# Kernel optimization log

Hardware: AMD Instinct MI355X
Metric: run time of the kernel (lower is better)

The kernel has to match this reference:

```python
import jax, jax.numpy as jnp
import numpy as np

ND, NPROT, E, L = 20000, 8000, 640000, 200000
DD, DP, H = 128, 128, 256

PARAM_SHAPES = {
    # conv_in, per edge type (dp: drug->protein writes into protein; pd: reverse)
    'Wl_in_dp': (DD, H), 'bl_in_dp': (H,), 'Wr_in_dp': (DP, H),
    'Wl_in_pd': (DP, H), 'bl_in_pd': (H,), 'Wr_in_pd': (DD, H),
    # conv_med (shared across the 2 middle iterations)
    'Wl_med_dp': (H, H), 'bl_med_dp': (H,), 'Wr_med_dp': (H, H),
    'Wl_med_pd': (H, H), 'bl_med_pd': (H,), 'Wr_med_pd': (H, H),
    # conv_out
    'Wl_out_dp': (H, H), 'bl_out_dp': (H,), 'Wr_out_dp': (H, H),
    'Wl_out_pd': (H, H), 'bl_out_pd': (H,), 'Wr_out_pd': (H, H),
    # edge decoder MLP
    'W1': (2 * H, H), 'b1': (H,), 'W2': (H, 1), 'b2': (1,),
}


def setup_inputs() -> dict:
    key = jax.random.key(0)
    ks = jax.random.split(key, 6 + len(PARAM_SHAPES))
    def nrm(k, shape):
        return jax.random.normal(k, shape, dtype=jnp.float32) * 0.05
    inp = {
        'x_drug': nrm(ks[0], (ND, DD)),
        'x_prot': nrm(ks[1], (NPROT, DP)),
        'ei_src': jax.random.randint(ks[2], (E,), 0, ND, dtype=jnp.int32),
        'ei_dst': jax.random.randint(ks[3], (E,), 0, NPROT, dtype=jnp.int32),
        'eli_row': jax.random.randint(ks[4], (L,), 0, ND, dtype=jnp.int32),
        'eli_col': jax.random.randint(ks[5], (L,), 0, NPROT, dtype=jnp.int32),
    }
    for i, (name, sh) in enumerate(PARAM_SHAPES.items()):
        inp[name] = nrm(ks[6 + i], sh)
    return inp


def _sage(x_src, x_dst, src, dst, Wl, bl, Wr, n_dst):
    # SAGEConv(aggr='sum'): lin_l(scatter_sum over neighbors) + lin_r(x_dst)
    agg = jax.ops.segment_sum(x_src[src], dst, num_segments=n_dst)  # [n_dst, F]
    return agg @ Wl + bl + x_dst @ Wr


def reference(x_drug, x_prot, ei_src, ei_dst, eli_row, eli_col,
              Wl_in_dp, bl_in_dp, Wr_in_dp, Wl_in_pd, bl_in_pd, Wr_in_pd,
              Wl_med_dp, bl_med_dp, Wr_med_dp, Wl_med_pd, bl_med_pd, Wr_med_pd,
              Wl_out_dp, bl_out_dp, Wr_out_dp, Wl_out_pd, bl_out_pd, Wr_out_pd,
              W1, b1, W2, b2):
    def hetero_layer(xd, xp, Wl_dp, bl_dp, Wr_dp, Wl_pd, bl_pd, Wr_pd):
        zp = _sage(xd, xp, ei_src, ei_dst, Wl_dp, bl_dp, Wr_dp, NPROT)
        zd = _sage(xp, xd, ei_dst, ei_src, Wl_pd, bl_pd, Wr_pd, ND)
        return zd, zp

    # conv_in + tanh (dropout is identity in eval)
    xd, xp = hetero_layer(x_drug, x_prot, Wl_in_dp, bl_in_dp, Wr_in_dp,
                          Wl_in_pd, bl_in_pd, Wr_in_pd)
    xd, xp = jnp.tanh(xd), jnp.tanh(xp)
    # conv_med applied twice with shared weights
    for _ in range(2):
        xd, xp = hetero_layer(xd, xp, Wl_med_dp, bl_med_dp, Wr_med_dp,
                              Wl_med_pd, bl_med_pd, Wr_med_pd)
        xd, xp = jnp.tanh(xd), jnp.tanh(xp)
    # conv_out, no activation
    zd, zp = hetero_layer(xd, xp, Wl_out_dp, bl_out_dp, Wr_out_dp,
                          Wl_out_pd, bl_out_pd, Wr_out_pd)

    # edge decoder: gather pair embeddings -> 2-layer MLP
    z = jnp.concatenate([zd[eli_row], zp[eli_col]], axis=-1)  # [L, 2H]
    h = jax.nn.relu(z @ W1 + b1)
    out = (h @ W2 + b2).reshape(-1)  # [L]
    return (zd, zp, out)
```

## Files before the change

### kernel.cpp

```cpp
#include <hip/hip_runtime.h>
#include <hip/hip_bf16.h>

#define ND 20000
#define NP 8000
#define NE 640000
#define NL 200000
#define DD 128
#define HH 256

typedef __attribute__((ext_vector_type(8))) short short8;
typedef __attribute__((ext_vector_type(4))) float f32x4;

__device__ inline float bflo(unsigned int u) {
    union { unsigned int u; float f; } x; x.u = u << 16; return x.f;
}
__device__ inline float bfhi(unsigned int u) {
    union { unsigned int u; float f; } x; x.u = u & 0xffff0000u; return x.f;
}
__device__ inline unsigned short f2b(float f) {
    union { float f; unsigned int u; } x; x.f = f;
    unsigned int r = x.u + 0x7fffu + ((x.u >> 16) & 1u);
    return (unsigned short)(r >> 16);
}

__global__ void k_hist(const int* __restrict__ src, const int* __restrict__ dst,
                       int* __restrict__ deg_d, int* __restrict__ deg_p) {
    int i = blockIdx.x * blockDim.x + threadIdx.x;
    if (i < NE) {
        atomicAdd(&deg_p[dst[i]], 1);
        atomicAdd(&deg_d[src[i]], 1);
    }
}

__global__ void k_scan(const int* __restrict__ deg, int* __restrict__ rowptr,
                       int* __restrict__ cursor, int n) {
    __shared__ int s[1024];
    const int t = threadIdx.x;
    const int chunk = (n + 1023) / 1024;
    const int lo = t * chunk;
    const int hi = min(n, lo + chunk);
    int local = 0;
    for (int i = lo; i < hi; ++i) local += deg[i];
    s[t] = local;
    __syncthreads();
    for (int off = 1; off < 1024; off <<= 1) {
        int v = (t >= off) ? s[t - off] : 0;
        __syncthreads();
        s[t] += v;
        __syncthreads();
    }
    int base = s[t] - local;
    for (int i = lo; i < hi; ++i) {
        rowptr[i] = base;
        cursor[i] = base;
        base += deg[i];
    }
    if (t == 1023) rowptr[n] = s[1023];
}

__global__ void k_fill(const int* __restrict__ src, const int* __restrict__ dst,
                       int* __restrict__ cur_p, int* __restrict__ cur_d,
                       int* __restrict__ csr_p, int* __restrict__ csr_d) {
    int i = blockIdx.x * blockDim.x + threadIdx.x;
    if (i < NE) {
        int s = src[i], d = dst[i];
        csr_p[atomicAdd(&cur_p[d], 1)] = s;
        csr_d[atomicAdd(&cur_d[s], 1)] = d;
    }
}

__global__ void k_f2b(const float* __restrict__ in, unsigned short* __restrict__ out, int n4) {
    int i = blockIdx.x * blockDim.x + threadIdx.x;
    if (i < n4) {
        float4 v = ((const float4*)in)[i];
        ushort4 o;
        o.x = f2b(v.x); o.y = f2b(v.y); o.z = f2b(v.z); o.w = f2b(v.w);
        ((ushort4*)out)[i] = o;
    }
}

struct WtD { const float* src; unsigned short* dst; int kbits; };
struct WtPack { WtD d[14]; };
__global__ void k_wt(WtPack p) {
    WtD d = p.d[blockIdx.y];
    const int K = 1 << d.kbits;
    int i = blockIdx.x * blockDim.x + threadIdx.x;
    if (i < 256 * K) {
        int nn = i >> d.kbits, k = i & (K - 1);
        d.dst[i] = f2b(d.src[k * 256 + nn]);
    }
}

__global__ void k_agg128(const unsigned short* __restrict__ x, const int* __restrict__ rowptr,
                         const int* __restrict__ idx, unsigned short* __restrict__ agg) {
    const int b = blockIdx.x, t = threadIdx.x;
    const int s = rowptr[b], e = rowptr[b + 1];
    float a0 = 0.f, a1 = 0.f;
    int j = s;
    for (; j + 1 < e; j += 2) {
        unsigned int u = *(const unsigned int*)(x + (size_t)idx[j] * 128 + 2 * t);
        unsigned int v = *(const unsigned int*)(x + (size_t)idx[j + 1] * 128 + 2 * t);
        a0 += bflo(u) + bflo(v);
        a1 += bfhi(u) + bfhi(v);
    }
    if (j < e) {
        unsigned int u = *(const unsigned int*)(x + (size_t)idx[j] * 128 + 2 * t);
        a0 += bflo(u); a1 += bfhi(u);
    }
    agg[(size_t)b * 128 + 2 * t]     = f2b(a0);
    agg[(size_t)b * 128 + 2 * t + 1] = f2b(a1);
}

__global__ void k_agg256(const unsigned short* __restrict__ x, const int* __restrict__ rowptr,
                         const int* __restrict__ idx, unsigned short* __restrict__ agg) {
    const int b = blockIdx.x, t = threadIdx.x;
    const int s = rowptr[b], e = rowptr[b + 1];
    float a0 = 0.f, a1 = 0.f, a2 = 0.f, a3 = 0.f;
    int j = s;
    for (; j + 1 < e; j += 2) {
        uint2 u = *(const uint2*)(x + (size_t)idx[j] * 256 + 4 * t);
        uint2 v = *(const uint2*)(x + (size_t)idx[j + 1] * 256 + 4 * t);
        a0 += bflo(u.x) + bflo(v.x);
        a1 += bfhi(u.x) + bfhi(v.x);
        a2 += bflo(u.y) + bflo(v.y);
        a3 += bfhi(u.y) + bfhi(v.y);
    }
    if (j < e) {
        uint2 u = *(const uint2*)(x + (size_t)idx[j] * 256 + 4 * t);
        a0 += bflo(u.x); a1 += bfhi(u.x); a2 += bflo(u.y); a3 += bfhi(u.y);
    }
    agg[(size_t)b * 256 + 4 * t]     = f2b(a0);
    agg[(size_t)b * 256 + 4 * t + 1] = f2b(a1);
    agg[(size_t)b * 256 + 4 * t + 2] = f2b(a2);
    agg[(size_t)b * 256 + 4 * t + 3] = f2b(a3);
}

__global__ __launch_bounds__(256)
void k_mgemm(int n,
             const unsigned short* __restrict__ A1, const unsigned short* __restrict__ W1t, int K1,
             const unsigned short* __restrict__ A2, const unsigned short* __restrict__ W2t, int K2,
             const float* __restrict__ bias, float* __restrict__ outF,
             unsigned short* __restrict__ outB, int act) {
    __shared__ short As[64][40];
    __shared__ short Bs[128][40];

    const int tid = threadIdx.x;
    const int w = tid >> 6, l = tid & 63;
    const int m16 = l & 15, kg = l >> 4;
    const int row0 = blockIdx.x * 64;
    const int col0 = blockIdx.y * 128;

    const f32x4 z4 = {0.f, 0.f, 0.f, 0.f};
    f32x4 acc[4][2];
#pragma unroll
    for (int i = 0; i < 4; ++i)
#pragma unroll
        for (int j = 0; j < 2; ++j) acc[i][j] = z4;

    for (int pass = 0; pass < 2; ++pass) {
        const unsigned short* A  = pass ? A2 : A1;
        const unsigned short* Wt = pass ? W2t : W1t;
        const int K = pass ? K2 : K1;
        if (A == nullptr) continue;
        for (int k0 = 0; k0 < K; k0 += 32) {
            {
                const int ar = tid >> 2, ac = (tid & 3) * 8;
                const int gr = row0 + ar;
                short8 v = {0, 0, 0, 0, 0, 0, 0, 0};
                if (gr < n) v = *(const short8*)(A + (size_t)gr * K + k0 + ac);
                *(short8*)&As[ar][ac] = v;
                *(short8*)&Bs[ar][ac] =
                    *(const short8*)(Wt + (size_t)(col0 + ar) * K + k0 + ac);
                *(short8*)&Bs[ar + 64][ac] =
                    *(const short8*)(Wt + (size_t)(col0 + ar + 64) * K + k0 + ac);
            }
            __syncthreads();
            short8 af[4];
#pragma unroll
            for (int i = 0; i < 4; ++i) af[i] = *(const short8*)&As[16 * i + m16][8 * kg];
#pragma unroll
            for (int j = 0; j < 2; ++j) {
                short8 bf = *(const short8*)&Bs[32 * w + 16 * j + m16][8 * kg];
#pragma unroll
                for (int i = 0; i < 4; ++i)
                    acc[i][j] = __builtin_amdgcn_mfma_f32_16x16x32_bf16(af[i], bf, acc[i][j], 0, 0, 0);
            }
            __syncthreads();
        }
    }

#pragma unroll
    for (int j = 0; j < 2; ++j) {
        const int gc = col0 + 32 * w + 16 * j + m16;
        const float bv = bias ? bias[gc] : 0.f;
#pragma unroll
        for (int i = 0; i < 4; ++i) {
#pragma unroll
            for (int r = 0; r < 4; ++r) {
                const int gr = row0 + 16 * i + 4 * kg + r;
                if (gr < n) {
                    float v = acc[i][j][r] + bv;
                    if (act) v = tanhf(v);
                    if (outF) outF[(size_t)gr * HH + gc] = v;
                    if (outB) outB[(size_t)gr * HH + gc] = f2b(v);
                }
            }
        }
    }
}

__global__ void k_decode(const unsigned short* __restrict__ Ab, const unsigned short* __restrict__ Bb,
                         const int* __restrict__ rows, const int* __restrict__ cols,
                         const float* __restrict__ W2, const float* __restrict__ b2,
                         float* __restrict__ out) {
    const int wid = (blockIdx.x * blockDim.x + threadIdx.x) >> 6;
    const int lane = threadIdx.x & 63;
    if (wid >= NL) return;
    const int r = rows[wid], c = cols[wid];
    uint2 ua = *(const uint2*)(Ab + (size_t)r * HH + 4 * lane);
    uint2 ub = *(const uint2*)(Bb + (size_t)c * HH + 4 * lane);
    float4 wv = *(const float4*)(W2 + 4 * lane);
    float s = fmaxf(bflo(ua.x) + bflo(ub.x), 0.f) * wv.x +
              fmaxf(bfhi(ua.x) + bfhi(ub.x), 0.f) * wv.y +
              fmaxf(bflo(ua.y) + bflo(ub.y), 0.f) * wv.z +
              fmaxf(bfhi(ua.y) + bfhi(ub.y), 0.f) * wv.w;
#pragma unroll
    for (int off = 32; off > 0; off >>= 1) s += __shfl_xor(s, off, 64);
    if (lane == 0) out[wid] = s + b2[0];
}

extern "C" void kernel_launch(void* const* d_in, const int* in_sizes, int n_in,
                              void* d_out, int out_size, void* d_ws, size_t ws_size,
                              hipStream_t stream) {
    const float* x_drug  = (const float*)d_in[0];
    const float* x_prot  = (const float*)d_in[1];
    const int*   ei_src  = (const int*)d_in[2];
    const int*   ei_dst  = (const int*)d_in[3];
    const int*   eli_row = (const int*)d_in[4];
    const int*   eli_col = (const int*)d_in[5];
    const float* Wl_in_dp  = (const float*)d_in[6];
    const float* bl_in_dp  = (const float*)d_in[7];
    const float* Wr_in_dp  = (const float*)d_in[8];
    const float* Wl_in_pd  = (const float*)d_in[9];
    const float* bl_in_pd  = (const float*)d_in[10];
    const float* Wr_in_pd  = (const float*)d_in[11];
    const float* Wl_med_dp = (const float*)d_in[12];
    const float* bl_med_dp = (const float*)d_in[13];
    const float* Wr_med_dp = (const float*)d_in[14];
    const float* Wl_med_pd = (const float*)d_in[15];
    const float* bl_med_pd = (const float*)d_in[16];
    const float* Wr_med_pd = (const float*)d_in[17];
    const float* Wl_out_dp = (const float*)d_in[18];
    const float* bl_out_dp = (const float*)d_in[19];
    const float* Wr_out_dp = (const float*)d_in[20];
    const float* Wl_out_pd = (const float*)d_in[21];
    const float* bl_out_pd = (const float*)d_in[22];
    const float* Wr_out_pd = (const float*)d_in[23];
    const float* W1 = (const float*)d_in[24];
    const float* b1 = (const float*)d_in[25];
    const float* W2 = (const float*)d_in[26];
    const float* b2 = (const float*)d_in[27];

    char* ws = (char*)d_ws;
    size_t off = 0;
    auto alloc = [&](size_t bytes) {
        void* p = ws + off;
        off = (off + bytes + 255) & ~(size_t)255;
        return p;
    };

    int* deg_p    = (int*)alloc((size_t)NP * 4);
    int* deg_d    = (int*)alloc((size_t)ND * 4);
    int* rowptr_p = (int*)alloc((size_t)(NP + 1) * 4);
    int* rowptr_d = (int*)alloc((size_t)(ND + 1) * 4);
    int* cur_p    = (int*)alloc((size_t)NP * 4);
    int* cur_d    = (int*)alloc((size_t)ND * 4);
    int* csr_p    = (int*)alloc((size_t)NE * 4);
    int* csr_d    = (int*)alloc((size_t)NE * 4);

    unsigned short* wt[14];
    const int kk[14] = {128,128,128,128, 256,256,256,256, 256,256,256,256, 256,256};
    for (int i = 0; i < 14; ++i) wt[i] = (unsigned short*)alloc((size_t)256 * kk[i] * 2);

    unsigned short* xdbf = (unsigned short*)alloc((size_t)ND * DD * 2);
    unsigned short* xpbf = (unsigned short*)alloc((size_t)NP * DD * 2);
    unsigned short* xd_a = (unsigned short*)alloc((size_t)ND * HH * 2);
    unsigned short* xd_b = (unsigned short*)alloc((size_t)ND * HH * 2);
    unsigned short* xp_a = (unsigned short*)alloc((size_t)NP * HH * 2);
    unsigned short* xp_b = (unsigned short*)alloc((size_t)NP * HH * 2);
    unsigned short* aggd = (unsigned short*)alloc((size_t)ND * HH * 2);
    unsigned short* aggp = (unsigned short*)alloc((size_t)NP * HH * 2);
    unsigned short* zdbf = (unsigned short*)alloc((size_t)ND * HH * 2);
    unsigned short* zpbf = (unsigned short*)alloc((size_t)NP * HH * 2);

    float* zd   = (float*)d_out;
    float* zp   = zd + (size_t)ND * HH;
    float* outv = zp + (size_t)NP * HH;

    const dim3 gD((ND + 63) / 64, 2);
    const dim3 gP((NP + 63) / 64, 2);

    hipMemsetAsync(deg_p, 0, (size_t)NP * 4, stream);
    hipMemsetAsync(deg_d, 0, (size_t)ND * 4, stream);
    k_hist<<<(NE + 255) / 256, 256, 0, stream>>>(ei_src, ei_dst, deg_d, deg_p);
    k_scan<<<1, 1024, 0, stream>>>(deg_p, rowptr_p, cur_p, NP);
    k_scan<<<1, 1024, 0, stream>>>(deg_d, rowptr_d, cur_d, ND);
    k_fill<<<(NE + 255) / 256, 256, 0, stream>>>(ei_src, ei_dst, cur_p, cur_d, csr_p, csr_d);

    k_f2b<<<(ND * DD / 4 + 255) / 256, 256, 0, stream>>>(x_drug, xdbf, ND * DD / 4);
    k_f2b<<<(NP * DD / 4 + 255) / 256, 256, 0, stream>>>(x_prot, xpbf, NP * DD / 4);
    {
        WtPack p;
        const float* src[14] = {Wl_in_dp, Wr_in_dp, Wl_in_pd, Wr_in_pd,
                                Wl_med_dp, Wr_med_dp, Wl_med_pd, Wr_med_pd,
                                Wl_out_dp, Wr_out_dp, Wl_out_pd, Wr_out_pd,
                                W1, W1 + (size_t)HH * HH};
        for (int i = 0; i < 14; ++i) {
            p.d[i].src = src[i];
            p.d[i].dst = wt[i];
            p.d[i].kbits = (kk[i] == 128) ? 7 : 8;
        }
        k_wt<<<dim3(256, 14), 256, 0, stream>>>(p);
    }

    k_agg128<<<NP, 64, 0, stream>>>(xdbf, rowptr_p, csr_p, aggp);
    k_agg128<<<ND, 64, 0, stream>>>(xpbf, rowptr_d, csr_d, aggd);
    k_mgemm<<<gP, 256, 0, stream>>>(NP, aggp, wt[0], 128, xpbf, wt[1], 128, bl_in_dp, nullptr, xp_a, 1);
    k_mgemm<<<gD, 256, 0, stream>>>(ND, aggd, wt[2], 128, xdbf, wt[3], 128, bl_in_pd, nullptr, xd_a, 1);

    k_agg256<<<NP, 64, 0, stream>>>(xd_a, rowptr_p, csr_p, aggp);
    k_agg256<<<ND, 64, 0, stream>>>(xp_a, rowptr_d, csr_d, aggd);
    k_mgemm<<<gP, 256, 0, stream>>>(NP, aggp, wt[4], 256, xp_a, wt[5], 256, bl_med_dp, nullptr, xp_b, 1);
    k_mgemm<<<gD, 256, 0, stream>>>(ND, aggd, wt[6], 256, xd_a, wt[7], 256, bl_med_pd, nullptr, xd_b, 1);

    k_agg256<<<NP, 64, 0, stream>>>(xd_b, rowptr_p, csr_p, aggp);
    k_agg256<<<ND, 64, 0, stream>>>(xp_b, rowptr_d, csr_d, aggd);
    k_mgemm<<<gP, 256, 0, stream>>>(NP, aggp, wt[4], 256, xp_b, wt[5], 256, bl_med_dp, nullptr, xp_a, 1);
    k_mgemm<<<gD, 256, 0, stream>>>(ND, aggd, wt[6], 256, xd_b, wt[7], 256, bl_med_pd, nullptr, xd_a, 1);

    k_agg256<<<NP, 64, 0, stream>>>(xd_a, rowptr_p, csr_p, aggp);
    k_agg256<<<ND, 64, 0, stream>>>(xp_a, rowptr_d, csr_d, aggd);
    k_mgemm<<<gP, 256, 0, stream>>>(NP, aggp, wt[8], 256, xp_a, wt[9], 256, bl_out_dp, zp, zpbf, 0);
    k_mgemm<<<gD, 256, 0, stream>>>(ND, aggd, wt[10], 256, xd_a, wt[11], 256, bl_out_pd, zd, zdbf, 0);

    k_mgemm<<<gD, 256, 0, stream>>>(ND, zdbf, wt[12], 256, nullptr, nullptr, 0,
                                    nullptr, nullptr, xd_b, 0);
    k_mgemm<<<gP, 256, 0, stream>>>(NP, zpbf, wt[13], 256, nullptr, nullptr, 0,
                                    b1, nullptr, xp_b, 0);
    k_decode<<<(NL + 3) / 4, 256, 0, stream>>>(xd_b, xp_b, eli_row, eli_col, W2, b2, outv);
}
```

Baseline: 750.6 us.

## Batch drug/protein kernels into single launches and widen GEMM tile to full N

Merges the paired drug-side and protein-side launches (scan, f32-to-bf16 conversion, aggregation, GEMM) into single kernels that pick a side by block index, roughly halving the launch count. The GEMM tile also changes from 64x128 to 64x256, so each block covers all 256 output columns and the A tile is loaded once rather than twice. In exchange each block holds twice as many accumulators and twice the B shared-memory tile, which may reduce occupancy, and the GEMM grid shrinks to about 440 blocks.

```diff
diff --git a/kernel.cpp b/kernel.cpp
--- a/kernel.cpp
+++ b/kernel.cpp
@@ -32,9 +32,14 @@
     }
 }
 
-__global__ void k_scan(const int* __restrict__ deg, int* __restrict__ rowptr,
-                       int* __restrict__ cursor, int n) {
+__global__ void k_scan2(const int* __restrict__ degA, int* __restrict__ rowA,
+                        int* __restrict__ curA, int nA,
+                        const int* __restrict__ degB, int* __restrict__ rowB,
+                        int* __restrict__ curB, int nB) {
     __shared__ int s[1024];
+    const int* deg; int* rowptr; int* cursor; int n;
+    if (blockIdx.x == 0) { deg = degA; rowptr = rowA; cursor = curA; n = nA; }
+    else                 { deg = degB; rowptr = rowB; cursor = curB; n = nB; }
     const int t = threadIdx.x;
     const int chunk = (n + 1023) / 1024;
     const int lo = t * chunk;
@@ -69,13 +74,18 @@
     }
 }
 
-__global__ void k_f2b(const float* __restrict__ in, unsigned short* __restrict__ out, int n4) {
+__global__ void k_f2b2(const float* __restrict__ a, unsigned short* __restrict__ oa, int n4a,
+                       const float* __restrict__ b, unsigned short* __restrict__ ob, int n4b) {
     int i = blockIdx.x * blockDim.x + threadIdx.x;
-    if (i < n4) {
-        float4 v = ((const float4*)in)[i];
-        ushort4 o;
-        o.x = f2b(v.x); o.y = f2b(v.y); o.z = f2b(v.z); o.w = f2b(v.w);
-        ((ushort4*)out)[i] = o;
+    if (i < n4a) {
+        float4 v = ((const float4*)a)[i];
+        ushort4 o; o.x = f2b(v.x); o.y = f2b(v.y); o.z = f2b(v.z); o.w = f2b(v.w);
+        ((ushort4*)oa)[i] = o;
+    } else if (i - n4a < n4b) {
+        int j = i - n4a;
+        float4 v = ((const float4*)b)[j];
+        ushort4 o; o.x = f2b(v.x); o.y = f2b(v.y); o.z = f2b(v.z); o.w = f2b(v.w);
+        ((ushort4*)ob)[j] = o;
     }
 }
 
@@ -91,75 +101,86 @@
     }
 }
 
-__global__ void k_agg128(const unsigned short* __restrict__ x, const int* __restrict__ rowptr,
-                         const int* __restrict__ idx, unsigned short* __restrict__ agg) {
-    const int b = blockIdx.x, t = threadIdx.x;
-    const int s = rowptr[b], e = rowptr[b + 1];
+struct ASide { const unsigned short* x; const int* rowptr; const int* idx;
+               unsigned short* agg; int n; };
+
+__global__ void k_agg2_128(ASide s0, ASide s1) {
+    ASide S; int b;
+    int bi = blockIdx.x;
+    if (bi < s0.n) { S = s0; b = bi; } else { S = s1; b = bi - s0.n; }
+    const int t = threadIdx.x;
+    const int s = S.rowptr[b], e = S.rowptr[b + 1];
     float a0 = 0.f, a1 = 0.f;
     int j = s;
     for (; j + 1 < e; j += 2) {
-        unsigned int u = *(const unsigned int*)(x + (size_t)idx[j] * 128 + 2 * t);
-        unsigned int v = *(const unsigned int*)(x + (size_t)idx[j + 1] * 128 + 2 * t);
+        unsigned int u = *(const unsigned int*)(S.x + (size_t)S.idx[j] * 128 + 2 * t);
+        unsigned int v = *(const unsigned int*)(S.x + (size_t)S.idx[j + 1] * 128 + 2 * t);
         a0 += bflo(u) + bflo(v);
         a1 += bfhi(u) + bfhi(v);
     }
     if (j < e) {
-        unsigned int u = *(const unsigned int*)(x + (size_t)idx[j] * 128 + 2 * t);
+        unsigned int u = *(const unsigned int*)(S.x + (size_t)S.idx[j] * 128 + 2 * t);
         a0 += bflo(u); a1 += bfhi(u);
     }
-    agg[(size_t)b * 128 + 2 * t]     = f2b(a0);
-    agg[(size_t)b * 128 + 2 * t + 1] = f2b(a1);
-}
-
-__global__ void k_agg256(const unsigned short* __restrict__ x, const int* __restrict__ rowptr,
-                         const int* __restrict__ idx, unsigned short* __restrict__ agg) {
-    const int b = blockIdx.x, t = threadIdx.x;
-    const int s = rowptr[b], e = rowptr[b + 1];
+    S.agg[(size_t)b * 128 + 2 * t]     = f2b(a0);
+    S.agg[(size_t)b * 128 + 2 * t + 1] = f2b(a1);
+}
+
+__global__ void k_agg2_256(ASide s0, ASide s1) {
+    ASide S; int b;
+    int bi = blockIdx.x;
+    if (bi < s0.n) { S = s0; b = bi; } else { S = s1; b = bi - s0.n; }
+    const int t = threadIdx.x;
+    const int s = S.rowptr[b], e = S.rowptr[b + 1];
     float a0 = 0.f, a1 = 0.f, a2 = 0.f, a3 = 0.f;
     int j = s;
     for (; j + 1 < e; j += 2) {
-        uint2 u = *(const uint2*)(x + (size_t)idx[j] * 256 + 4 * t);
-        uint2 v = *(const uint2*)(x + (size_t)idx[j + 1] * 256 + 4 * t);
+        uint2 u = *(const uint2*)(S.x + (size_t)S.idx[j] * 256 + 4 * t);
+        uint2 v = *(const uint2*)(S.x + (size_t)S.idx[j + 1] * 256 + 4 * t);
         a0 += bflo(u.x) + bflo(v.x);
         a1 += bfhi(u.x) + bfhi(v.x);
         a2 += bflo(u.y) + bflo(v.y);
         a3 += bfhi(u.y) + bfhi(v.y);
     }
     if (j < e) {
-        uint2 u = *(const uint2*)(x + (size_t)idx[j] * 256 + 4 * t);
+        uint2 u = *(const uint2*)(S.x + (size_t)S.idx[j] * 256 + 4 * t);
         a0 += bflo(u.x); a1 += bfhi(u.x); a2 += bflo(u.y); a3 += bfhi(u.y);
     }
-    agg[(size_t)b * 256 + 4 * t]     = f2b(a0);
-    agg[(size_t)b * 256 + 4 * t + 1] = f2b(a1);
-    agg[(size_t)b * 256 + 4 * t + 2] = f2b(a2);
-    agg[(size_t)b * 256 + 4 * t + 3] = f2b(a3);
-}
+    S.agg[(size_t)b * 256 + 4 * t]     = f2b(a0);
+    S.agg[(size_t)b * 256 + 4 * t + 1] = f2b(a1);
+    S.agg[(size_t)b * 256 + 4 * t + 2] = f2b(a2);
+    S.agg[(size_t)b * 256 + 4 * t + 3] = f2b(a3);
+}
+
+struct GSide { const unsigned short* A1; const unsigned short* W1t;
+               const unsigned short* A2; const unsigned short* W2t;
+               const float* bias; float* outF; unsigned short* outB; int n; };
 
 __global__ __launch_bounds__(256)
-void k_mgemm(int n,
-             const unsigned short* __restrict__ A1, const unsigned short* __restrict__ W1t, int K1,
-             const unsigned short* __restrict__ A2, const unsigned short* __restrict__ W2t, int K2,
-             const float* __restrict__ bias, float* __restrict__ outF,
-             unsigned short* __restrict__ outB, int act) {
+void k_mgemm2(GSide s0, GSide s1, int nblk0, int K1, int K2, int act) {
     __shared__ short As[64][40];
-    __shared__ short Bs[128][40];
+    __shared__ short Bs[256][40];
+
+    GSide S;
+    int bx;
+    if ((int)blockIdx.x < nblk0) { S = s0; bx = blockIdx.x; }
+    else                          { S = s1; bx = blockIdx.x - nblk0; }
 
     const int tid = threadIdx.x;
     const int w = tid >> 6, l = tid & 63;
     const int m16 = l & 15, kg = l >> 4;
-    const int row0 = blockIdx.x * 64;
-    const int col0 = blockIdx.y * 128;
+    const int row0 = bx * 64;
 
     const f32x4 z4 = {0.f, 0.f, 0.f, 0.f};
-    f32x4 acc[4][2];
+    f32x4 acc[4][4];
 #pragma unroll
     for (int i = 0; i < 4; ++i)
 #pragma unroll
-        for (int j = 0; j < 2; ++j) acc[i][j] = z4;
+        for (int j = 0; j < 4; ++j) acc[i][j] = z4;
 
     for (int pass = 0; pass < 2; ++pass) {
-        const unsigned short* A  = pass ? A2 : A1;
-        const unsigned short* Wt = pass ? W2t : W1t;
+        const unsigned short* A  = pass ? S.A2 : S.A1;
+        const unsigned short* Wt = pass ? S.W2t : S.W1t;
         const int K = pass ? K2 : K1;
         if (A == nullptr) continue;
         for (int k0 = 0; k0 < K; k0 += 32) {
@@ -167,20 +188,20 @@
                 const int ar = tid >> 2, ac = (tid & 3) * 8;
                 const int gr = row0 + ar;
                 short8 v = {0, 0, 0, 0, 0, 0, 0, 0};
-                if (gr < n) v = *(const short8*)(A + (size_t)gr * K + k0 + ac);
+                if (gr < S.n) v = *(const short8*)(A + (size_t)gr * K + k0 + ac);
                 *(short8*)&As[ar][ac] = v;
-                *(short8*)&Bs[ar][ac] =
-                    *(const short8*)(Wt + (size_t)(col0 + ar) * K + k0 + ac);
-                *(short8*)&Bs[ar + 64][ac] =
-                    *(const short8*)(Wt + (size_t)(col0 + ar + 64) * K + k0 + ac);
+#pragma unroll
+                for (int h = 0; h < 4; ++h)
+                    *(short8*)&Bs[ar + 64 * h][ac] =
+                        *(const short8*)(Wt + (size_t)(ar + 64 * h) * K + k0 + ac);
             }
             __syncthreads();
             short8 af[4];
 #pragma unroll
             for (int i = 0; i < 4; ++i) af[i] = *(const short8*)&As[16 * i + m16][8 * kg];
 #pragma unroll
-            for (int j = 0; j < 2; ++j) {
-                short8 bf = *(const short8*)&Bs[32 * w + 16 * j + m16][8 * kg];
+            for (int j = 0; j < 4; ++j) {
+                short8 bf = *(const short8*)&Bs[64 * w + 16 * j + m16][8 * kg];
 #pragma unroll
                 for (int i = 0; i < 4; ++i)
                     acc[i][j] = __builtin_amdgcn_mfma_f32_16x16x32_bf16(af[i], bf, acc[i][j], 0, 0, 0);
@@ -190,19 +211,19 @@
     }
 
 #pragma unroll
-    for (int j = 0; j < 2; ++j) {
-        const int gc = col0 + 32 * w + 16 * j + m16;
-        const float bv = bias ? bias[gc] : 0.f;
+    for (int j = 0; j < 4; ++j) {
+        const int gc = 64 * w + 16 * j + m16;
+        const float bv = S.bias ? S.bias[gc] : 0.f;
 #pragma unroll
         for (int i = 0; i < 4; ++i) {
 #pragma unroll
             for (int r = 0; r < 4; ++r) {
                 const int gr = row0 + 16 * i + 4 * kg + r;
-                if (gr < n) {
+                if (gr < S.n) {
                     float v = acc[i][j][r] + bv;
                     if (act) v = tanhf(v);
-                    if (outF) outF[(size_t)gr * HH + gc] = v;
-                    if (outB) outB[(size_t)gr * HH + gc] = f2b(v);
+                    if (S.outF) S.outF[(size_t)gr * HH + gc] = v;
+                    if (S.outB) S.outB[(size_t)gr * HH + gc] = f2b(v);
                 }
             }
         }
@@ -297,18 +318,20 @@
     float* zp   = zd + (size_t)ND * HH;
     float* outv = zp + (size_t)NP * HH;
 
-    const dim3 gD((ND + 63) / 64, 2);
-    const dim3 gP((NP + 63) / 64, 2);
+    const int nbD = (ND + 63) / 64;
+    const int nbP = (NP + 63) / 64;
+    const dim3 gG(nbD + nbP);
+    const dim3 gA(NP + ND);
 
     hipMemsetAsync(deg_p, 0, (size_t)NP * 4, stream);
     hipMemsetAsync(deg_d, 0, (size_t)ND * 4, stream);
     k_hist<<<(NE + 255) / 256, 256, 0, stream>>>(ei_src, ei_dst, deg_d, deg_p);
-    k_scan<<<1, 1024, 0, stream>>>(deg_p, rowptr_p, cur_p, NP);
-    k_scan<<<1, 1024, 0, stream>>>(deg_d, rowptr_d, cur_d, ND);
+    k_scan2<<<2, 1024, 0, stream>>>(deg_p, rowptr_p, cur_p, NP,
+                                    deg_d, rowptr_d, cur_d, ND);
     k_fill<<<(NE + 255) / 256, 256, 0, stream>>>(ei_src, ei_dst, cur_p, cur_d, csr_p, csr_d);
 
-    k_f2b<<<(ND * DD / 4 + 255) / 256, 256, 0, stream>>>(x_drug, xdbf, ND * DD / 4);
-    k_f2b<<<(NP * DD / 4 + 255) / 256, 256, 0, stream>>>(x_prot, xpbf, NP * DD / 4);
+    k_f2b2<<<(ND * DD / 4 + NP * DD / 4 + 255) / 256, 256, 0, stream>>>(
+        x_drug, xdbf, ND * DD / 4, x_prot, xpbf, NP * DD / 4);
     {
         WtPack p;
         const float* src[14] = {Wl_in_dp, Wr_in_dp, Wl_in_pd, Wr_in_pd,
@@ -323,29 +346,47 @@
         k_wt<<<dim3(256, 14), 256, 0, stream>>>(p);
     }
 
-    k_agg128<<<NP, 64, 0, stream>>>(xdbf, rowptr_p, csr_p, aggp);
-    k_agg128<<<ND, 64, 0, stream>>>(xpbf, rowptr_d, csr_d, aggd);
-    k_mgemm<<<gP, 256, 0, stream>>>(NP, aggp, wt[0], 128, xpbf, wt[1], 128, bl_in_dp, nullptr, xp_a, 1);
-    k_mgemm<<<gD, 256, 0, stream>>>(ND, aggd, wt[2], 128, xdbf, wt[3], 128, bl_in_pd, nullptr, xd_a, 1);
-
-    k_agg256<<<NP, 64, 0, stream>>>(xd_a, rowptr_p, csr_p, aggp);
-    k_agg256<<<ND, 64, 0, stream>>>(xp_a, rowptr_d, csr_d, aggd);
-    k_mgemm<<<gP, 256, 0, stream>>>(NP, aggp, wt[4], 256, xp_a, wt[5], 256, bl_med_dp, nullptr, xp_b, 1);
-    k_mgemm<<<gD, 256, 0, stream>>>(ND, aggd, wt[6], 256, xd_a, wt[7], 256, bl_med_pd, nullptr, xd_b, 1);
-
-    k_agg256<<<NP, 64, 0, stream>>>(xd_b, rowptr_p, csr_p, aggp);
-    k_agg256<<<ND, 64, 0, stream>>>(xp_b, rowptr_d, csr_d, aggd);
-    k_mgemm<<<gP, 256, 0, stream>>>(NP, aggp, wt[4], 256, xp_b, wt[5], 256, bl_med_dp, nullptr, xp_a, 1);
-    k_mgemm<<<gD, 256, 0, stream>>>(ND, aggd, wt[6], 256, xd_b, wt[7], 256, bl_med_pd, nullptr, xd_a, 1);
-
-    k_agg256<<<NP, 64, 0, stream>>>(xd_a, rowptr_p, csr_p, aggp);
-    k_agg256<<<ND, 64, 0, stream>>>(xp_a, rowptr_d, csr_d, aggd);
-    k_mgemm<<<gP, 256, 0, stream>>>(NP, aggp, wt[8], 256, xp_a, wt[9], 256, bl_out_dp, zp, zpbf, 0);
-    k_mgemm<<<gD, 256, 0, stream>>>(ND, aggd, wt[10], 256, xd_a, wt[11], 256, bl_out_pd, zd, zdbf, 0);
-
-    k_mgemm<<<gD, 256, 0, stream>>>(ND, zdbf, wt[12], 256, nullptr, nullptr, 0,
-                                    nullptr, nullptr, xd_b, 0);
-    k_mgemm<<<gP, 256, 0, stream>>>(NP, zpbf, wt[13], 256, nullptr, nullptr, 0,
-                                    b1, nullptr, xp_b, 0);
+    ASide aP128 = {xdbf, rowptr_p, csr_p, aggp, NP};
+    ASide aD128 = {xpbf, rowptr_d, csr_d, aggd, ND};
+
+    k_agg2_128<<<gA, 64, 0, stream>>>(aP128, aD128);
+    {
+        GSide d = {aggd, wt[2], xdbf, wt[3], bl_in_pd, nullptr, xd_a, ND};
+        GSide pS = {aggp, wt[0], xpbf, wt[1], bl_in_dp, nullptr, xp_a, NP};
+        k_mgemm2<<<gG, 256, 0, stream>>>(d, pS, nbD, 128, 128, 1);
+    }
+
+    {
+        ASide aP = {xd_a, rowptr_p, csr_p, aggp, NP};
+        ASide aD = {xp_a, rowptr_d, csr_d, aggd, ND};
+        k_agg2_256<<<gA, 64, 0, stream>>>(aP, aD);
+        GSide d = {aggd, wt[6], xd_a, wt[7], bl_med_pd, nullptr, xd_b, ND};
+        GSide pS = {aggp, wt[4], xp_a, wt[5], bl_med_dp, nullptr, xp_b, NP};
+        k_mgemm2<<<gG, 256, 0, stream>>>(d, pS, nbD, 256, 256, 1);
+    }
+
+    {
+        ASide aP = {xd_b, rowptr_p, csr_p, aggp, NP};
+        ASide aD = {xp_b, rowptr_d, csr_d, aggd, ND};
+        k_agg2_256<<<gA, 64, 0, stream>>>(aP, aD);
+        GSide d = {aggd, wt[6], xd_b, wt[7], bl_med_pd, nullptr, xd_a, ND};
+        GSide pS = {aggp, wt[4], xp_b, wt[5], bl_med_dp, nullptr, xp_a, NP};
+        k_mgemm2<<<gG, 256, 0, stream>>>(d, pS, nbD, 256, 256, 1);
+    }
+
+    {
+        ASide aP = {xd_a, rowptr_p, csr_p, aggp, NP};
+        ASide aD = {xp_a, rowptr_d, csr_d, aggd, ND};
+        k_agg2_256<<<gA, 64, 0, stream>>>(aP, aD);
+        GSide d = {aggd, wt[10], xd_a, wt[11], bl_out_pd, zd, zdbf, ND};
+        GSide pS = {aggp, wt[8], xp_a, wt[9], bl_out_dp, zp, zpbf, NP};
+        k_mgemm2<<<gG, 256, 0, stream>>>(d, pS, nbD, 256, 256, 0);
+    }
+
+    {
+        GSide d = {zdbf, wt[12], nullptr, nullptr, nullptr, nullptr, xd_b, ND};
+        GSide pS = {zpbf, wt[13], nullptr, nullptr, b1, nullptr, xp_b, NP};
+        k_mgemm2<<<gG, 256, 0, stream>>>(d, pS, nbD, 256, 256, 0);
+    }
     k_decode<<<(NL + 3) / 4, 256, 0, stream>>>(xd_b, xp_b, eli_row, eli_col, W2, b2, outv);
 }
```

Result: faster. 683.9 us (-8.9%).
